# Kernel tuning notes

Measured on AMD Instinct MI355X. Metric: run time of the kernel, lower is better.

## Reference

```python
import jax, jax.numpy as jnp
import numpy as np

WAY = 5
SHOT = 5
SCALE = 10.0
EPS = 1e-8


def setup_inputs() -> dict:
    key = jax.random.key(0)
    k1, k2 = jax.random.split(key, 2)
    x = jax.random.normal(k1, (100, 512, 16, 16), dtype=jnp.float32)
    W = jax.random.normal(k2, (512, 512), dtype=jnp.float32) * 0.02  # 1x1 conv weight (outC, inC)
    b = jnp.zeros((512,), dtype=jnp.float32)
    return {"x": x, "W": W, "b": b}


def reference(x, W, b):
    B, C, H, Wd = x.shape
    # extract(): 1x1 conv -> softmax over flattened (C*H*W) per sample -> remask
    mask = jnp.einsum('bchw,oc->bohw', x, W) + b[None, :, None, None]
    mask = jax.nn.softmax(mask.reshape(B, -1), axis=1).reshape(B, C, H, Wd)
    x = x * mask
    # predict(): (way, shot+query, C, H, W)
    xv = x.reshape(WAY, -1, C, H, Wd)
    s = xv[:, :SHOT].mean(axis=(1, 3, 4))                    # (m=way, d=C) support prototypes
    q = xv[:, SHOT:].reshape(-1, C, H * Wd)                  # (n, d=C, f=H*W) queries
    # cosine_similarity over d, without materializing (n,m,d,f)
    qn = jnp.maximum(jnp.sqrt(jnp.sum(q * q, axis=1)), EPS)  # (n, f)
    sn = jnp.maximum(jnp.sqrt(jnp.sum(s * s, axis=1)), EPS)  # (m,)
    scores = jnp.einsum('ndf,md->nmf', q, s) / (qn[:, None, :] * sn[None, :, None])
    # softmax over classes (m), then mean over spatial positions f
    return jax.nn.softmax(SCALE * scores, axis=1).mean(axis=2)  # (n, way)
```

## Files before the change

### kernel.cpp

```cpp
#include <hip/hip_runtime.h>
#include <hip/hip_bf16.h>
#include <math.h>

typedef _Float16 half8 __attribute__((ext_vector_type(8)));
typedef float f32x4 __attribute__((ext_vector_type(4)));

#define BATCH 100
#define CH    512
#define HWP   256
#define SAMP  (CH * HWP)

__device__ __forceinline__ void async16(const void* g, void* l) {
  __builtin_amdgcn_global_load_lds(
      (const __attribute__((address_space(1))) unsigned int*)g,
      (__attribute__((address_space(3))) unsigned int*)l, 16, 0, 0);
}

__global__ __launch_bounds__(256) void k_txpose(const float* __restrict__ x,
                                               _Float16* __restrict__ xh,
                                               const float* __restrict__ W,
                                               _Float16* __restrict__ Wh) {
  int bid = blockIdx.x;
  int t = threadIdx.x;
  if (bid >= 3200) {
    int base = (bid - 3200) * 1024 + t;
#pragma unroll
    for (int j = 0; j < 4; j++) Wh[base + j * 256] = (_Float16)W[base + j * 256];
    return;
  }
  __shared__ float tb[64][69];
  int b    = bid >> 5;
  int tile = bid & 31;
  int c0 = (tile >> 2) << 6;
  int p0 = (tile & 3) << 6;
  const float* xb = x + (size_t)b * SAMP;
#pragma unroll
  for (int it = 0; it < 4; it++) {
    int ch = it * 256 + t;
    int c  = ch >> 4;
    int pc = (ch & 15) << 2;
    float4 v = *(const float4*)(xb + (size_t)(c0 + c) * HWP + p0 + pc);
    tb[c][pc] = v.x; tb[c][pc + 1] = v.y; tb[c][pc + 2] = v.z; tb[c][pc + 3] = v.w;
  }
  __syncthreads();
  _Float16* xhb = xh + (size_t)b * SAMP;
#pragma unroll
  for (int it = 0; it < 2; it++) {
    int ch = it * 256 + t;
    int p  = ch >> 3;
    int ck = (ch & 7) << 3;
    half8 h;
#pragma unroll
    for (int j = 0; j < 8; j++) h[j] = (_Float16)tb[ck + j][p];
    *(half8*)(xhb + (size_t)(p0 + p) * CH + c0 + ck) = h;
  }
}

__global__ __launch_bounds__(256) void k_gemm(const _Float16* __restrict__ Wh,
                                             const _Float16* __restrict__ xh,
                                             const float* __restrict__ bias,
                                             _Float16* __restrict__ u,
                                             float* __restrict__ denom) {
  __shared__ __align__(16) _Float16 As[128 * 32];
  __shared__ __align__(16) _Float16 Bs[128 * 32];
  __shared__ __align__(16) _Float16 xk[128 * 136];
  __shared__ float rs[4];
  int bid   = blockIdx.x;
  int batch = bid >> 3;
  int sub   = bid & 7;
  int ot = sub & 3, pt = sub >> 2;
  int o0 = ot * 128, p0 = pt * 128;
  const _Float16* Bg = xh + (size_t)batch * SAMP;

  int t  = threadIdx.x;
  int wv = t >> 6, ln = t & 63;
  int qd = ln >> 4, r = ln & 15;
  int wm0 = (wv >> 1) * 64, wn0 = (wv & 1) * 64;

  f32x4 acc[4][4] = {};

  for (int kk = 0; kk < 512; kk += 32) {
#pragma unroll
    for (int it = 0; it < 2; it++) {
      int ch  = it * 256 + t;
      int row = ch >> 2;
      int qc  = ch & 3;
      char* la = (char*)As + (size_t)(it * 256 + wv * 64) * 16;
      char* lb = (char*)Bs + (size_t)(it * 256 + wv * 64) * 16;
      async16((const char*)(Wh + (size_t)(o0 + row) * 512 + kk + qc * 8), la);
      async16((const char*)(Bg + (size_t)(p0 + row) * 512 + kk + qc * 8), lb);
    }
    if ((unsigned)(kk - o0) < 128u) {
      int ko = kk - o0;
#pragma unroll
      for (int it = 0; it < 2; it++) {
        int ch  = it * 256 + t;
        int row = ch >> 2;
        int qc  = ch & 3;
        half8 v = *(const half8*)(Bg + (size_t)(p0 + row) * 512 + kk + qc * 8);
        *(half8*)(xk + row * 136 + ko + qc * 8) = v;
      }
    }
    __syncthreads();
    half8 af[4], bf[4];
#pragma unroll
    for (int i = 0; i < 4; i++)
      af[i] = *(const half8*)(As + (wm0 + i * 16 + r) * 32 + qd * 8);
#pragma unroll
    for (int j = 0; j < 4; j++)
      bf[j] = *(const half8*)(Bs + (wn0 + j * 16 + r) * 32 + qd * 8);
#pragma unroll
    for (int i = 0; i < 4; i++)
#pragma unroll
      for (int j = 0; j < 4; j++)
        acc[i][j] = __builtin_amdgcn_mfma_f32_16x16x32_f16(af[i], bf[j], acc[i][j], 0, 0, 0);
    __syncthreads();
  }

  float lsum = 0.f;
#pragma unroll
  for (int i = 0; i < 4; i++) {
#pragma unroll
    for (int rg = 0; rg < 4; rg++) {
      int ol = wm0 + i * 16 + qd * 4 + rg;
      float bv = bias[o0 + ol];
#pragma unroll
      for (int j = 0; j < 4; j++) {
        int pl = wn0 + j * 16 + r;
        float ev = __expf(acc[i][j][rg] + bv);
        lsum += ev;
        acc[i][j][rg] = (float)xk[pl * 136 + ol] * ev;
      }
    }
  }
#pragma unroll
  for (int off = 32; off; off >>= 1) lsum += __shfl_down(lsum, off, 64);
  if (ln == 0) rs[wv] = lsum;
  __syncthreads();
  if (t == 0) atomicAdd(&denom[batch], rs[0] + rs[1] + rs[2] + rs[3]);

#pragma unroll
  for (int i = 0; i < 4; i++)
#pragma unroll
    for (int rg = 0; rg < 4; rg++) {
      int ol = wm0 + i * 16 + qd * 4 + rg;
#pragma unroll
      for (int j = 0; j < 4; j++) {
        int pl = wn0 + j * 16 + r;
        xk[ol * 136 + pl] = (_Float16)acc[i][j][rg];
      }
    }
  __syncthreads();

  _Float16* outb = u + (size_t)batch * SAMP + (size_t)o0 * HWP + p0;
#pragma unroll
  for (int it = 0; it < 8; it++) {
    int ch  = it * 256 + t;
    int row = ch >> 4;
    int ck  = ch & 15;
    half8 v = *(const half8*)(xk + row * 136 + ck * 8);
    *(half8*)(outb + (size_t)row * HWP + ck * 8) = v;
  }
}

__global__ __launch_bounds__(256) void k_proto(const _Float16* __restrict__ u,
                                              const float* __restrict__ denom,
                                              float* __restrict__ sproto) {
  int m = blockIdx.x / 512, c = blockIdx.x % 512;
  int t = threadIdx.x;
  float acc = 0.f;
  for (int j = 0; j < 5; j++) {
    int b = m * 20 + j;
    float invd = 1.0f / denom[b];
    acc += (float)u[(size_t)b * SAMP + (size_t)c * HWP + t] * invd;
  }
#pragma unroll
  for (int off = 32; off; off >>= 1) acc += __shfl_down(acc, off, 64);
  __shared__ float rs[4];
  if ((t & 63) == 0) rs[t >> 6] = acc;
  __syncthreads();
  if (t == 0) sproto[m * 512 + c] = (rs[0] + rs[1] + rs[2] + rs[3]) * (1.0f / 1280.0f);
}

__global__ __launch_bounds__(256) void k_part(const _Float16* __restrict__ u,
                                             const float* __restrict__ sproto,
                                             float* __restrict__ part) {
  __shared__ float s_l[5 * 64];
  int n = blockIdx.x >> 3, gc = blockIdx.x & 7;
  int b = (n / 15) * 20 + 5 + (n % 15);
  int t = threadIdx.x;
  for (int i = t; i < 320; i += 256)
    s_l[i] = sproto[(i >> 6) * 512 + gc * 64 + (i & 63)];
  __syncthreads();
  const _Float16* ub = u + (size_t)b * SAMP + (size_t)gc * 64 * HWP;
  float dot[5] = {0, 0, 0, 0, 0}, qq = 0.f;
#pragma unroll 8
  for (int c = 0; c < 64; c++) {
    float v = (float)ub[c * HWP + t];
    qq += v * v;
#pragma unroll
    for (int m = 0; m < 5; m++) dot[m] += v * s_l[m * 64 + c];
  }
  float* pp = part + (((size_t)n * 8 + gc) * 256 + t) * 6;
  pp[0] = dot[0]; pp[1] = dot[1]; pp[2] = dot[2];
  pp[3] = dot[3]; pp[4] = dot[4]; pp[5] = qq;
}

__global__ __launch_bounds__(256) void k_comb(const float* __restrict__ part,
                                             const float* __restrict__ sproto,
                                             float* __restrict__ out) {
  __shared__ float prefs[5];
  int n = blockIdx.x, t = threadIdx.x;
  int wvi = t >> 6, ln = t & 63;
  for (int m = wvi; m < 5; m += 4) {
    float a = 0.f;
    for (int i = ln; i < 512; i += 64) { float v = sproto[m * 512 + i]; a += v * v; }
#pragma unroll
    for (int off = 32; off; off >>= 1) a += __shfl_down(a, off, 64);
    if (ln == 0) prefs[m] = 10.0f / fmaxf(sqrtf(a), 1e-8f);
  }
  __syncthreads();
  float dot[5] = {0, 0, 0, 0, 0}, qq = 0.f;
#pragma unroll
  for (int gc = 0; gc < 8; gc++) {
    const float* pp = part + (((size_t)n * 8 + gc) * 256 + t) * 6;
    dot[0] += pp[0]; dot[1] += pp[1]; dot[2] += pp[2];
    dot[3] += pp[3]; dot[4] += pp[4]; qq += pp[5];
  }
  float iqn = 1.0f / fmaxf(sqrtf(qq), 1e-20f);
  float sc[5], mx = -1e30f;
#pragma unroll
  for (int m = 0; m < 5; m++) { sc[m] = dot[m] * prefs[m] * iqn; mx = fmaxf(mx, sc[m]); }
  float p[5], ssum = 0.f;
#pragma unroll
  for (int m = 0; m < 5; m++) { p[m] = __expf(sc[m] - mx); ssum += p[m]; }
  float rr = 1.0f / ssum;
#pragma unroll
  for (int m = 0; m < 5; m++) {
    float v = p[m] * rr;
#pragma unroll
    for (int off = 32; off; off >>= 1) v += __shfl_down(v, off, 64);
    p[m] = v;
  }
  __shared__ float rsb[4][5];
  if (ln == 0) {
#pragma unroll
    for (int m = 0; m < 5; m++) rsb[wvi][m] = p[m];
  }
  __syncthreads();
  if (t < 5) out[n * 5 + t] =
      (rsb[0][t] + rsb[1][t] + rsb[2][t] + rsb[3][t]) * (1.0f / 256.0f);
}

extern "C" void kernel_launch(void* const* d_in, const int* in_sizes, int n_in,
                              void* d_out, int out_size, void* d_ws, size_t ws_size,
                              hipStream_t stream) {
  const float* x    = (const float*)d_in[0];
  const float* W    = (const float*)d_in[1];
  const float* bias = (const float*)d_in[2];
  float* out = (float*)d_out;

  char* ws = (char*)d_ws;
  _Float16* xh     = (_Float16*)(ws + 0);
  float*    part   = (float*)   (ws + 0);
  _Float16* Wh     = (_Float16*)(ws + 26214400);
  _Float16* u      = (_Float16*)(ws + 26738688);
  float*    denom  = (float*)   (ws + 52953088);
  float*    sproto = (float*)   (ws + 52953600);

  hipMemsetAsync(denom, 0, 512, stream);
  k_txpose <<<3456, 256, 0, stream>>>(x, xh, W, Wh);
  k_gemm   <<<800,  256, 0, stream>>>(Wh, xh, bias, u, denom);
  k_proto  <<<2560, 256, 0, stream>>>(u, denom, sproto);
  k_part   <<<600,  256, 0, stream>>>(u, sproto, part);
  k_comb   <<<75,   256, 0, stream>>>(part, sproto, out);
}
```

Baseline: 143.4 us.

## Fuse x transpose and fp16 conversion into GEMM B-tile loading

Removes the separate transpose kernel that wrote an fp16 channel-last copy of x. The GEMM now reads fp32 x directly, converts it to fp16 and scatters it transposed into a padded LDS tile, and also fills the xk capture buffer. This saves a full write and re-read of a 26MB intermediate and one launch. In exchange, the GEMM loses async global-to-LDS loads for B, issues more scalar LDS stores, and each x tile is read by four output-tile blocks in fp32, which doubles the bytes per element read.

Result: slower. 173.8 us (+21.2%).

```diff
diff --git a/kernel.cpp b/kernel.cpp
--- a/kernel.cpp
+++ b/kernel.cpp
@@ -3,12 +3,14 @@
 #include <math.h>
 
 typedef _Float16 half8 __attribute__((ext_vector_type(8)));
+typedef _Float16 half4 __attribute__((ext_vector_type(4)));
 typedef float f32x4 __attribute__((ext_vector_type(4)));
 
 #define BATCH 100
 #define CH    512
 #define HWP   256
 #define SAMP  (CH * HWP)
+#define BSR   36
 
 __device__ __forceinline__ void async16(const void* g, void* l) {
   __builtin_amdgcn_global_load_lds(
@@ -16,53 +18,20 @@
       (__attribute__((address_space(3))) unsigned int*)l, 16, 0, 0);
 }
 
-__global__ __launch_bounds__(256) void k_txpose(const float* __restrict__ x,
-                                               _Float16* __restrict__ xh,
-                                               const float* __restrict__ W,
-                                               _Float16* __restrict__ Wh) {
-  int bid = blockIdx.x;
-  int t = threadIdx.x;
-  if (bid >= 3200) {
-    int base = (bid - 3200) * 1024 + t;
-#pragma unroll
-    for (int j = 0; j < 4; j++) Wh[base + j * 256] = (_Float16)W[base + j * 256];
-    return;
-  }
-  __shared__ float tb[64][69];
-  int b    = bid >> 5;
-  int tile = bid & 31;
-  int c0 = (tile >> 2) << 6;
-  int p0 = (tile & 3) << 6;
-  const float* xb = x + (size_t)b * SAMP;
-#pragma unroll
-  for (int it = 0; it < 4; it++) {
-    int ch = it * 256 + t;
-    int c  = ch >> 4;
-    int pc = (ch & 15) << 2;
-    float4 v = *(const float4*)(xb + (size_t)(c0 + c) * HWP + p0 + pc);
-    tb[c][pc] = v.x; tb[c][pc + 1] = v.y; tb[c][pc + 2] = v.z; tb[c][pc + 3] = v.w;
-  }
-  __syncthreads();
-  _Float16* xhb = xh + (size_t)b * SAMP;
-#pragma unroll
-  for (int it = 0; it < 2; it++) {
-    int ch = it * 256 + t;
-    int p  = ch >> 3;
-    int ck = (ch & 7) << 3;
-    half8 h;
-#pragma unroll
-    for (int j = 0; j < 8; j++) h[j] = (_Float16)tb[ck + j][p];
-    *(half8*)(xhb + (size_t)(p0 + p) * CH + c0 + ck) = h;
-  }
+__global__ __launch_bounds__(256) void k_convw(const float* __restrict__ W,
+                                              _Float16* __restrict__ Wh) {
+  int base = blockIdx.x * 1024 + threadIdx.x;
+#pragma unroll
+  for (int j = 0; j < 4; j++) Wh[base + j * 256] = (_Float16)W[base + j * 256];
 }
 
 __global__ __launch_bounds__(256) void k_gemm(const _Float16* __restrict__ Wh,
-                                             const _Float16* __restrict__ xh,
+                                             const float* __restrict__ x,
                                              const float* __restrict__ bias,
                                              _Float16* __restrict__ u,
                                              float* __restrict__ denom) {
   __shared__ __align__(16) _Float16 As[128 * 32];
-  __shared__ __align__(16) _Float16 Bs[128 * 32];
+  __shared__ __align__(16) _Float16 Bs[128 * BSR];
   __shared__ __align__(16) _Float16 xk[128 * 136];
   __shared__ float rs[4];
   int bid   = blockIdx.x;
@@ -70,12 +39,15 @@
   int sub   = bid & 7;
   int ot = sub & 3, pt = sub >> 2;
   int o0 = ot * 128, p0 = pt * 128;
-  const _Float16* Bg = xh + (size_t)batch * SAMP;
+  const float* xb = x + (size_t)batch * SAMP;
 
   int t  = threadIdx.x;
   int wv = t >> 6, ln = t & 63;
   int qd = ln >> 4, r = ln & 15;
   int wm0 = (wv >> 1) * 64, wn0 = (wv & 1) * 64;
+
+  int crA = (t >> 5) * 8;
+  int pg  = t & 31;
 
   f32x4 acc[4][4] = {};
 
@@ -86,19 +58,26 @@
       int row = ch >> 2;
       int qc  = ch & 3;
       char* la = (char*)As + (size_t)(it * 256 + wv * 64) * 16;
-      char* lb = (char*)Bs + (size_t)(it * 256 + wv * 64) * 16;
       async16((const char*)(Wh + (size_t)(o0 + row) * 512 + kk + qc * 8), la);
-      async16((const char*)(Bg + (size_t)(p0 + row) * 512 + kk + qc * 8), lb);
-    }
-    if ((unsigned)(kk - o0) < 128u) {
-      int ko = kk - o0;
-#pragma unroll
-      for (int it = 0; it < 2; it++) {
-        int ch  = it * 256 + t;
-        int row = ch >> 2;
-        int qc  = ch & 3;
-        half8 v = *(const half8*)(Bg + (size_t)(p0 + row) * 512 + kk + qc * 8);
-        *(half8*)(xk + row * 136 + ko + qc * 8) = v;
+    }
+    bool cap = (unsigned)(kk - o0) < 128u;
+#pragma unroll
+    for (int pass = 0; pass < 4; pass++) {
+      int cr = (t >> 5) + pass * 8;
+      float4 v = *(const float4*)(xb + (size_t)(kk + cr) * HWP + p0 + pg * 4);
+      _Float16 h0 = (_Float16)v.x, h1 = (_Float16)v.y,
+               h2 = (_Float16)v.z, h3 = (_Float16)v.w;
+      int p4 = pg * 4;
+      Bs[(p4 + 0) * BSR + cr] = h0;
+      Bs[(p4 + 1) * BSR + cr] = h1;
+      Bs[(p4 + 2) * BSR + cr] = h2;
+      Bs[(p4 + 3) * BSR + cr] = h3;
+      if (cap) {
+        int ol = kk + cr - o0;
+        xk[(p4 + 0) * 136 + ol] = h0;
+        xk[(p4 + 1) * 136 + ol] = h1;
+        xk[(p4 + 2) * 136 + ol] = h2;
+        xk[(p4 + 3) * 136 + ol] = h3;
       }
     }
     __syncthreads();
@@ -107,8 +86,12 @@
     for (int i = 0; i < 4; i++)
       af[i] = *(const half8*)(As + (wm0 + i * 16 + r) * 32 + qd * 8);
 #pragma unroll
-    for (int j = 0; j < 4; j++)
-      bf[j] = *(const half8*)(Bs + (wn0 + j * 16 + r) * 32 + qd * 8);
+    for (int j = 0; j < 4; j++) {
+      const _Float16* bp = Bs + (wn0 + j * 16 + r) * BSR + qd * 8;
+      half4 lo = *(const half4*)bp;
+      half4 hi = *(const half4*)(bp + 4);
+      bf[j] = half8{lo[0], lo[1], lo[2], lo[3], hi[0], hi[1], hi[2], hi[3]};
+    }
 #pragma unroll
     for (int i = 0; i < 4; i++)
 #pragma unroll
@@ -261,16 +244,15 @@
   float* out = (float*)d_out;
 
   char* ws = (char*)d_ws;
-  _Float16* xh     = (_Float16*)(ws + 0);
   float*    part   = (float*)   (ws + 0);
-  _Float16* Wh     = (_Float16*)(ws + 26214400);
-  _Float16* u      = (_Float16*)(ws + 26738688);
-  float*    denom  = (float*)   (ws + 52953088);
-  float*    sproto = (float*)   (ws + 52953600);
+  _Float16* Wh     = (_Float16*)(ws + 4194304);
+  _Float16* u      = (_Float16*)(ws + 8388608);
+  float*    denom  = (float*)   (ws + 34603008);
+  float*    sproto = (float*)   (ws + 34603520);
 
   hipMemsetAsync(denom, 0, 512, stream);
-  k_txpose <<<3456, 256, 0, stream>>>(x, xh, W, Wh);
-  k_gemm   <<<800,  256, 0, stream>>>(Wh, xh, bias, u, denom);
+  k_convw  <<<256,  256, 0, stream>>>(W, Wh);
+  k_gemm   <<<800,  256, 0, stream>>>(Wh, x, bias, u, denom);
   k_proto  <<<2560, 256, 0, stream>>>(u, denom, sproto);
   k_part   <<<600,  256, 0, stream>>>(u, sproto, part);
   k_comb   <<<75,   256, 0, stream>>>(part, sproto, out);
```
